# Performance work log

Measured on AMD Instinct MI355X. Metric: run time of the kernel, lower is better.

The kernel has to match this reference:

```python
import jax, jax.numpy as jnp
import numpy as np

N = 100000      # nodes
E = 1600000     # edges (before self-loops)
DIM = 128       # input feature dim
H = 5           # attention heads
C = 10          # per-head output channels
G = 256         # graphs in batch
NEG_SLOPE = 0.2 # PyG GATConv default


def setup_inputs() -> dict:
    key = jax.random.key(0)
    ks = jax.random.split(key, 8)
    x = jax.random.normal(ks[0], (N, DIM), jnp.float32)
    edge_index = jax.random.randint(ks[1], (2, E), 0, N, dtype=jnp.int64)
    batch = jnp.sort(jax.random.randint(ks[2], (N,), 0, G, dtype=jnp.int64))
    W = jax.random.normal(ks[3], (DIM, H * C), jnp.float32) * 0.05
    att_src = jax.random.normal(ks[4], (H, C), jnp.float32) * 0.1
    att_dst = jax.random.normal(ks[5], (H, C), jnp.float32) * 0.1
    bias = jnp.zeros((H * C,), jnp.float32)
    lin_w = jax.random.normal(ks[6], (H * C, 1), jnp.float32) * 0.1
    lin_b = jnp.zeros((1,), jnp.float32)
    return {"x": x, "W": W, "att_src": att_src, "att_dst": att_dst,
            "bias": bias, "lin_w": lin_w, "lin_b": lin_b,
            "edge_index": edge_index, "batch": batch}


def reference(x, W, att_src, att_dst, bias, lin_w, lin_b, edge_index, batch):
    n = x.shape[0]
    # PyG GATConv adds self-loops by default
    loop = jnp.arange(n, dtype=edge_index.dtype)
    src = jnp.concatenate([edge_index[0], loop])  # message sources j
    dst = jnp.concatenate([edge_index[1], loop])  # message targets i

    xw = (x @ W).reshape(n, H, C)                       # [N,H,C]
    a_src = jnp.einsum('nhc,hc->nh', xw, att_src)       # [N,H]
    a_dst = jnp.einsum('nhc,hc->nh', xw, att_dst)       # [N,H]

    logits = jax.nn.leaky_relu(a_src[src] + a_dst[dst], NEG_SLOPE)  # [Etot,H]
    # segment softmax over incoming edges per target node
    m = jax.ops.segment_max(logits, dst, num_segments=n)
    ex = jnp.exp(logits - m[dst])
    denom = jax.ops.segment_sum(ex, dst, num_segments=n)
    alpha = ex / denom[dst]                              # [Etot,H]

    msg = alpha[:, :, None] * xw[src]                    # [Etot,H,C]
    out = jax.ops.segment_sum(msg, dst, num_segments=n).reshape(n, H * C) + bias
    out = jax.nn.elu(out)                                # [N,H*C]

    # global_mean_pool over graph ids
    gsum = jax.ops.segment_sum(out, batch, num_segments=G)
    cnt = jax.ops.segment_sum(jnp.ones((n,), out.dtype), batch, num_segments=G)
    h = gsum / jnp.maximum(cnt, 1.0)[:, None]            # [G,H*C]

    # dropout p=0.5 is identity at inference (training=False)
    y = jax.nn.sigmoid(h @ lin_w + lin_b)                # [G,1]
    return (h, y)
```

## Files before the change

### kernel.cpp

```cpp
#include <hip/hip_runtime.h>
#include <hip/hip_bf16.h>
#include <hip/hip_fp8.h>
#include <math.h>

#define DIM 128
#define H 5
#define C 10
#define HC 50
#define NG 256
#define NEG_SLOPE 0.2f
#define UNR 8
#define WP 136
#define LOG2E 1.4426950408889634f

#define BSH 6
#define NB 1563
#define SB_CAP 1344
#define B1_BLOCKS 196
#define B1_CHUNK 8192

#define BKN2 32
#define ROWS_LDS2 (BKN2 * 64)

typedef short short8 __attribute__((ext_vector_type(8)));
typedef float floatx4 __attribute__((ext_vector_type(4)));
typedef float floatx2 __attribute__((ext_vector_type(2)));

__device__ inline short f2bf(float f) {
  __hip_bfloat16 h = __float2bfloat16(f);
  return *reinterpret_cast<short*>(&h);
}
#if __has_builtin(__builtin_amdgcn_cvt_f32_fp8)
__device__ inline float fp8tof(int b) { return __builtin_amdgcn_cvt_f32_fp8(b, 0); }
#else
__device__ inline float fp8tof(int b) {
  __hip_fp8_e4m3 v;
  v.__x = (__hip_fp8_storage_t)b;
  return (float)v;
}
#endif
#if __has_builtin(__builtin_amdgcn_cvt_pk_f32_fp8)
__device__ inline floatx2 fp8pk2(int us) {
  return __builtin_amdgcn_cvt_pk_f32_fp8(us, false);
}
#else
__device__ inline floatx2 fp8pk2(int us) {
  floatx2 r;
  r.x = fp8tof(us & 0xff);
  r.y = fp8tof((us >> 8) & 0xff);
  return r;
}
#endif
#if __has_builtin(__builtin_amdgcn_exp2f)
__device__ inline float fexp2(float x) { return __builtin_amdgcn_exp2f(x); }
#else
__device__ inline float fexp2(float x) { return exp2f(x); }
#endif
#if __has_builtin(__builtin_amdgcn_cvt_pk_fp8_f32)
__device__ inline unsigned ftofp8pk(float a, float b) {
  return (unsigned)__builtin_amdgcn_cvt_pk_fp8_f32(a, b, 0, false) & 0xffffu;
}
__device__ inline unsigned char ftofp8(float f) {
  return (unsigned char)(ftofp8pk(f, f) & 0xff);
}
#else
__device__ inline unsigned char ftofp8(float f) {
  __hip_fp8_e4m3 v(f);
  return v.__x;
}
__device__ inline unsigned ftofp8pk(float a, float b) {
  return (unsigned)ftofp8(a) | ((unsigned)ftofp8(b) << 8);
}
#endif

__global__ void k_zero(int* __restrict__ g, unsigned char* __restrict__ recb,
                       int n) {
  int t = blockIdx.x * blockDim.x + threadIdx.x;
  if (t < NB) g[t] = 0;
  if (blockIdx.x == 1 && threadIdx.x < 64)
    recb[((size_t)n << 6) + threadIdx.x] = (threadIdx.x < HC) ? 0x00 : 0xFE;
}

__global__ __launch_bounds__(256) void k_work(
    const int* __restrict__ src, const int* __restrict__ dst,
    int* __restrict__ gcur, int* __restrict__ seg,
    const float* __restrict__ x, const float* __restrict__ W,
    const float* __restrict__ att_src, const float* __restrict__ att_dst,
    unsigned char* __restrict__ recb, __hip_bfloat16* __restrict__ adst,
    int E_, int n) {
  __shared__ __align__(16) char smem[NB * 3 * sizeof(int)];
  int tid = threadIdx.x;
  if (blockIdx.x < B1_BLOCKS) {
    int* hist = (int*)smem;
    int* curs = hist + NB;
    int* baser = curs + NB;
    for (int i = tid; i < NB; i += 256) hist[i] = 0;
    __syncthreads();
    int e0 = blockIdx.x * B1_CHUNK;
    int dreg[32];
#pragma unroll
    for (int k = 0; k < 32; ++k) {
      int e = e0 + (k << 8) + tid;
      dreg[k] = (e < E_) ? dst[e] : -1;
      if (dreg[k] >= 0) atomicAdd(&hist[((unsigned)dreg[k]) >> BSH], 1);
    }
    __syncthreads();
    for (int i = tid; i < NB; i += 256) {
      baser[i] = hist[i] ? atomicAdd(&gcur[i], hist[i]) : 0;
      curs[i] = 0;
    }
    __syncthreads();
#pragma unroll
    for (int k = 0; k < 32; ++k) {
      if (dreg[k] >= 0) {
        int d = dreg[k];
        int s = ((unsigned)d) >> BSH;
        int pos = baser[s] + atomicAdd(&curs[s], 1);
        if (pos < SB_CAP)
          seg[(size_t)s * SB_CAP + pos] = (src[e0 + (k << 8) + tid] << 6) | (d & 63);
      }
    }
    return;
  }
  short* swt = (short*)smem;
  {
    int k = tid & 127;
    if (tid < 128) {
      for (int j = 0; j < HC; ++j) swt[j * WP + k] = f2bf(W[k * HC + j]);
    } else {
      float sv[H] = {0.f, 0.f, 0.f, 0.f, 0.f};
      float dv[H] = {0.f, 0.f, 0.f, 0.f, 0.f};
#pragma unroll
      for (int c = 0; c < HC; ++c) {
        float w = W[k * HC + c];
        sv[c / C] += w * att_src[c];
        dv[c / C] += w * att_dst[c];
      }
#pragma unroll
      for (int h = 0; h < H; ++h) {
        swt[(HC + h) * WP + k] = f2bf(sv[h] * LOG2E);
        swt[(55 + h) * WP + k] = f2bf(dv[h] * LOG2E);
      }
      for (int j = 60; j < 64; ++j) swt[j * WP + k] = 0;
    }
  }
  __syncthreads();
  int wv = tid >> 6, lane = tid & 63;
  int tiles = (n + 15) >> 4;
  int tile = (blockIdx.x - B1_BLOCKS) * 4 + wv;
  if (tile >= tiles) return;
  int r = lane & 15, q = lane >> 4;
  int node = tile * 16 + r;
  const float* xr = x + (size_t)min(node, n - 1) * DIM + q * 8;
  floatx4 acc[4];
#pragma unroll
  for (int nt = 0; nt < 4; ++nt) acc[nt] = (floatx4){0.f, 0.f, 0.f, 0.f};
#pragma unroll
  for (int ks = 0; ks < 4; ++ks) {
    float4 a0 = *(const float4*)(xr + ks * 32);
    float4 a1 = *(const float4*)(xr + ks * 32 + 4);
    short8 bx;
    bx[0] = f2bf(a0.x); bx[1] = f2bf(a0.y); bx[2] = f2bf(a0.z); bx[3] = f2bf(a0.w);
    bx[4] = f2bf(a1.x); bx[5] = f2bf(a1.y); bx[6] = f2bf(a1.z); bx[7] = f2bf(a1.w);
    const short* wb = &swt[r * WP + q * 8 + ks * 32];
    short8 w0 = *(const short8*)(wb);
    short8 w1 = *(const short8*)(wb + 16 * WP);
    short8 w2 = *(const short8*)(wb + 32 * WP);
    short8 w3 = *(const short8*)(wb + 48 * WP);
    acc[0] = __builtin_amdgcn_mfma_f32_16x16x32_bf16(w0, bx, acc[0], 0, 0, 0);
    acc[1] = __builtin_amdgcn_mfma_f32_16x16x32_bf16(w1, bx, acc[1], 0, 0, 0);
    acc[2] = __builtin_amdgcn_mfma_f32_16x16x32_bf16(w2, bx, acc[2], 0, 0, 0);
    acc[3] = __builtin_amdgcn_mfma_f32_16x16x32_bf16(w3, bx, acc[3], 0, 0, 0);
  }
  float xa = __shfl_up(acc[3][3], 16);
  float xb = __shfl_up(acc[3][1], 16);
  float xc = __shfl_up(acc[3][2], 16);
  if (node < n) {
    size_t base = (size_t)node << 6;
#pragma unroll
    for (int nt = 0; nt < 3; ++nt) {
      unsigned d = ftofp8pk(acc[nt][0], acc[nt][1]) |
                   (ftofp8pk(acc[nt][2], acc[nt][3]) << 16);
      *(unsigned*)(recb + base + nt * 16 + (q << 2)) = d;
    }
    unsigned d;
    if (q == 0) {
      d = ftofp8pk(acc[3][0], acc[3][1]) | (ftofp8pk(acc[3][2], acc[3][2]) << 16);
    } else if (q == 1) {
      d = ftofp8pk(xa, xa) | (ftofp8pk(acc[3][0], acc[3][0]) << 16);
      adst[(size_t)node * H + 0] = __float2bfloat16(acc[3][3]);
    } else if (q == 2) {
      d = ftofp8pk(xb, xb) | (ftofp8pk(xc, xc) << 16);
      adst[(size_t)node * H + 1] = __float2bfloat16(acc[3][0]);
      adst[(size_t)node * H + 2] = __float2bfloat16(acc[3][1]);
      adst[(size_t)node * H + 3] = __float2bfloat16(acc[3][2]);
      adst[(size_t)node * H + 4] = __float2bfloat16(acc[3][3]);
    } else {
      d = 0;
    }
    *(unsigned*)(recb + base + 48 + (q << 2)) = d;
  }
}

__global__ __launch_bounds__(256) void k_bin_gat(
    const int* __restrict__ seg, const int* __restrict__ gcur,
    const unsigned char* __restrict__ recb, const __hip_bfloat16* __restrict__ adst,
    const float* __restrict__ bias, float* __restrict__ out_node, int n) {
  __shared__ int rows[ROWS_LDS2];
  __shared__ __align__(16) int wbuf[4][128];
  int tid = threadIdx.x;
  int blk = blockIdx.x;
  int b = blk >> 1;
  int half32 = blk & 1;
  int lo = (b << BSH) + (half32 << 5);
  int hi = min(lo + BKN2, n);
  for (int k = tid; k < ROWS_LDS2; k += 256) rows[k] = n;
  __syncthreads();
  int cnt = min(gcur[b], SB_CAP);
  for (int k = tid; k < cnt; k += 256) {
    int e = seg[(size_t)b * SB_CAP + k];
    int dl = e & 63;
    if ((dl >> 5) == half32) {
      int s = ((unsigned)e) >> 6;
      int base = (dl & 31) << 6;
      int off = s & 63;
      int old = atomicExch(&rows[base + off], s);
      int probes = 0;
      while (old != n && probes < 128) {
        off = (off + 1) & 63;
        old = atomicExch(&rows[base + off], old);
        ++probes;
      }
    }
  }
  __syncthreads();

  int w = tid >> 6, lane = tid & 63;
  int* wb = wbuf[w];
  int nn = hi - lo;
  int pairsN = (nn + 1) >> 1;
  int hl = lane & 31;
  int hf = lane >> 5;
  bool chl = hl < 25;
  int h = hl / 5;
  int bpidx = ((hf << 5) + 25 + h) << 2;
  unsigned rowoff = (unsigned)(hl << 1);
  int rbase = hf << 6;

  for (int pr = w; pr < pairsN; pr += 4) {
    int i0l = pr * 2;
    int i1l = min(i0l + 1, nn - 1);
    int i0 = lo + i0l, i1 = lo + i1l;
    int iown = hf ? i1 : i0;
    float adi = 0.f;
    if (chl) adi = __bfloat162float(adst[(size_t)iown * H + h]);

    int jraw0 = rows[(i0l << 6) | lane];
    int jraw1 = rows[(i1l << 6) | lane];
    ((int2*)wb)[lane] = make_int2(n, n);
    bool v0 = (unsigned)jraw0 < (unsigned)n;
    unsigned long long mk0 = __ballot(v0);
    int deg0 = __popcll(mk0);
    int bel0 = __popcll(mk0 & ((1ull << lane) - 1ull));
    if (v0) wb[bel0] = jraw0;
    bool v1 = (unsigned)jraw1 < (unsigned)n;
    unsigned long long mk1 = __ballot(v1);
    int deg1 = __popcll(mk1);
    int bel1 = __popcll(mk1 & ((1ull << lane) - 1ull));
    if (v1) wb[64 + bel1] = jraw1;
    int mx = max(deg0, deg1);

    float dpA, dpB = 0.f, a0A, a0B = 0.f, a1A, a1B = 0.f;
    {
      int us = *(const unsigned short*)(recb + (((size_t)(unsigned)iown << 6) | rowoff));
      int asv = __builtin_amdgcn_ds_bpermute(bpidx, us);
      float asi = fp8tof(asv);
      float z = asi + adi;
      z = fmaxf(z, NEG_SLOPE * z);
      float pw = fexp2(z);
      floatx2 f = fp8pk2(us);
      dpA = pw;
      a0A = pw * f.x;
      a1A = pw * f.y;
    }
    for (int s0 = 0; s0 < mx; s0 += UNR) {
      int2 jp[UNR / 2];
#pragma unroll
      for (int up = 0; up < UNR / 2; ++up)
        jp[up] = *(const int2*)&wb[rbase + s0 + up * 2];
#pragma unroll
      for (int u = 0; u < UNR; ++u) {
        unsigned j = (unsigned)((u & 1) ? jp[u >> 1].y : jp[u >> 1].x);
        int us = *(const unsigned short*)(recb + (((size_t)j << 6) | rowoff));
        int asv = __builtin_amdgcn_ds_bpermute(bpidx, us);
        float asi = fp8tof(asv);
        float z = asi + adi;
        z = fmaxf(z, NEG_SLOPE * z);
        float pw = fexp2(z);
        floatx2 f = fp8pk2(us);
        if (u & 1) {
          dpB += pw;
          a0B = fmaf(pw, f.x, a0B);
          a1B = fmaf(pw, f.y, a1B);
        } else {
          dpA += pw;
          a0A = fmaf(pw, f.x, a0A);
          a1A = fmaf(pw, f.y, a1A);
        }
      }
    }
    if (chl) {
      float dp = dpA + dpB;
      float a0 = a0A + a0B, a1 = a1A + a1B;
      int c0 = hl * 2;
      float o0 = a0 / dp + bias[c0];
      o0 = o0 > 0.f ? o0 : __expf(o0) - 1.f;
      float o1 = a1 / dp + bias[c0 + 1];
      o1 = o1 > 0.f ? o1 : __expf(o1) - 1.f;
      float2 st;
      st.x = o0;
      st.y = o1;
      *(float2*)(out_node + (size_t)iown * HC + c0) = st;
    }
  }
}

__global__ __launch_bounds__(1024) void k_pool(
    const float* __restrict__ out_node, const int* __restrict__ batch,
    const float* __restrict__ lin_w, const float* __restrict__ lin_b,
    float* __restrict__ out, int n) {
  __shared__ int sb[2];
  __shared__ float sacc[16][HC];
  int g = blockIdx.x;
  int t = threadIdx.x;
  if (t < 2) {
    int target = g + t, lo = 0, hi = n;
    while (lo < hi) {
      int mid = (lo + hi) >> 1;
      if (batch[mid] < target) lo = mid + 1; else hi = mid;
    }
    sb[t] = lo;
  }
  __syncthreads();
  int s = sb[0], e = sb[1];
  int w = t >> 6, lane = t & 63;
  float a = 0.f;
  if (lane < HC)
    for (int i = s + w; i < e; i += 16) a += out_node[(size_t)i * HC + lane];
  if (lane < HC) sacc[w][lane] = a;
  __syncthreads();
  if (t < HC) {
    float r0 = 0.f, r1 = 0.f, r2 = 0.f, r3 = 0.f;
#pragma unroll
    for (int k = 0; k < 4; ++k) {
      r0 += sacc[k][t];
      r1 += sacc[4 + k][t];
      r2 += sacc[8 + k][t];
      r3 += sacc[12 + k][t];
    }
    float hv = ((r0 + r1) + (r2 + r3)) / fmaxf((float)(e - s), 1.f);
    out[g * HC + t] = hv;
    sacc[0][t] = hv * lin_w[t];
  }
  __syncthreads();
  if (t == 0) {
    float p = 0.f;
    for (int c = 0; c < HC; ++c) p += sacc[0][c];
    out[NG * HC + g] = 1.f / (1.f + __expf(-(p + lin_b[0])));
  }
}

extern "C" void kernel_launch(void* const* d_in, const int* in_sizes, int n_in,
                              void* d_out, int out_size, void* d_ws, size_t ws_size,
                              hipStream_t stream) {
  const float* x       = (const float*)d_in[0];
  const float* W       = (const float*)d_in[1];
  const float* att_src = (const float*)d_in[2];
  const float* att_dst = (const float*)d_in[3];
  const float* bias    = (const float*)d_in[4];
  const float* lin_w   = (const float*)d_in[5];
  const float* lin_b   = (const float*)d_in[6];
  const int*   eidx    = (const int*)d_in[7];
  const int*   batch   = (const int*)d_in[8];

  int n  = in_sizes[0] / DIM;
  int E_ = in_sizes[7] / 2;
  const int* srcp = eidx;
  const int* dstp = eidx + E_;

  char* p = (char*)d_ws;
  float* out_node = (float*)p; p += (size_t)n * HC * sizeof(float);
  unsigned char* recb = (unsigned char*)p; p += (size_t)(n + 1) * 64;
  __hip_bfloat16* adst = (__hip_bfloat16*)p; p += (size_t)n * H * sizeof(__hip_bfloat16);
  p = (char*)(((uintptr_t)p + 255) & ~(uintptr_t)255);
  int* gcur = (int*)p; p += NB * sizeof(int);
  p = (char*)(((uintptr_t)p + 255) & ~(uintptr_t)255);
  int* seg = (int*)p; p += (size_t)NB * SB_CAP * sizeof(int);

  float* out = (float*)d_out;

  int tiles = (n + 15) / 16;
  int mfma_blocks = (tiles + 3) / 4;
  int nbk2 = (n + BKN2 - 1) / BKN2;

  k_zero<<<2, 1024, 0, stream>>>(gcur, recb, n);
  k_work<<<B1_BLOCKS + mfma_blocks, 256, 0, stream>>>(
      srcp, dstp, gcur, seg, x, W, att_src, att_dst, recb, adst, E_, n);
  k_bin_gat<<<nbk2, 256, 0, stream>>>(seg, gcur, recb, adst, bias, out_node, n);
  k_pool<<<NG, 1024, 0, stream>>>(out_node, batch, lin_w, lin_b, out, n);
}
```

Baseline: 200.6 us.

## Replace global-atomic bucket cursors with per-block fixed-slot bucket storage

The edge binning pass no longer reserves space in each bucket with global atomics on a shared cursor array. Each binning block now writes its edges into private fixed-size slots per bucket, along with a per-block count, and the number of binning blocks is doubled with half-size chunks. The aggregation kernel then walks every block's slot list for its bucket. This removes global atomic contention and the need to zero the counters, but adds many scattered small reads in the aggregation kernel, a much larger sparse segment buffer, and silently drops edges when a block puts more than the slot count into one bucket.

```diff
diff --git a/kernel.cpp b/kernel.cpp
--- a/kernel.cpp
+++ b/kernel.cpp
@@ -15,9 +15,9 @@
 
 #define BSH 6
 #define NB 1563
-#define SB_CAP 1344
-#define B1_BLOCKS 196
-#define B1_CHUNK 8192
+#define B1_BLOCKS 391
+#define B1_CHUNK 4096
+#define SLOTS 24
 
 #define BKN2 32
 #define ROWS_LDS2 (BKN2 * 64)
@@ -73,51 +73,46 @@
 }
 #endif
 
-__global__ void k_zero(int* __restrict__ g, unsigned char* __restrict__ recb,
-                       int n) {
-  int t = blockIdx.x * blockDim.x + threadIdx.x;
-  if (t < NB) g[t] = 0;
-  if (blockIdx.x == 1 && threadIdx.x < 64)
+__global__ void k_zero(unsigned char* __restrict__ recb, int n) {
+  if (threadIdx.x < 64)
     recb[((size_t)n << 6) + threadIdx.x] = (threadIdx.x < HC) ? 0x00 : 0xFE;
 }
 
 __global__ __launch_bounds__(256) void k_work(
     const int* __restrict__ src, const int* __restrict__ dst,
-    int* __restrict__ gcur, int* __restrict__ seg,
+    int* __restrict__ cnts, int* __restrict__ seg,
     const float* __restrict__ x, const float* __restrict__ W,
     const float* __restrict__ att_src, const float* __restrict__ att_dst,
     unsigned char* __restrict__ recb, __hip_bfloat16* __restrict__ adst,
     int E_, int n) {
-  __shared__ __align__(16) char smem[NB * 3 * sizeof(int)];
+  __shared__ __align__(16) char smem[64 * WP * sizeof(short)];
   int tid = threadIdx.x;
   if (blockIdx.x < B1_BLOCKS) {
     int* hist = (int*)smem;
-    int* curs = hist + NB;
-    int* baser = curs + NB;
+    int blk = blockIdx.x;
     for (int i = tid; i < NB; i += 256) hist[i] = 0;
     __syncthreads();
-    int e0 = blockIdx.x * B1_CHUNK;
-    int dreg[32];
-#pragma unroll
-    for (int k = 0; k < 32; ++k) {
+    int e0 = blk * B1_CHUNK;
+    int dreg[16];
+#pragma unroll
+    for (int k = 0; k < 16; ++k) {
       int e = e0 + (k << 8) + tid;
       dreg[k] = (e < E_) ? dst[e] : -1;
       if (dreg[k] >= 0) atomicAdd(&hist[((unsigned)dreg[k]) >> BSH], 1);
     }
     __syncthreads();
-    for (int i = tid; i < NB; i += 256) {
-      baser[i] = hist[i] ? atomicAdd(&gcur[i], hist[i]) : 0;
-      curs[i] = 0;
-    }
+    for (int i = tid; i < NB; i += 256)
+      cnts[blk * NB + i] = min(hist[i], SLOTS);
     __syncthreads();
 #pragma unroll
-    for (int k = 0; k < 32; ++k) {
+    for (int k = 0; k < 16; ++k) {
       if (dreg[k] >= 0) {
         int d = dreg[k];
         int s = ((unsigned)d) >> BSH;
-        int pos = baser[s] + atomicAdd(&curs[s], 1);
-        if (pos < SB_CAP)
-          seg[(size_t)s * SB_CAP + pos] = (src[e0 + (k << 8) + tid] << 6) | (d & 63);
+        int pos = atomicAdd(&hist[s], -1) - 1;
+        if (pos >= 0 && pos < SLOTS)
+          seg[(size_t)(blk * NB + s) * SLOTS + pos] =
+              (src[e0 + (k << 8) + tid] << 6) | (d & 63);
       }
     }
     return;
@@ -203,7 +198,7 @@
 }
 
 __global__ __launch_bounds__(256) void k_bin_gat(
-    const int* __restrict__ seg, const int* __restrict__ gcur,
+    const int* __restrict__ cnts, const int* __restrict__ seg,
     const unsigned char* __restrict__ recb, const __hip_bfloat16* __restrict__ adst,
     const float* __restrict__ bias, float* __restrict__ out_node, int n) {
   __shared__ int rows[ROWS_LDS2];
@@ -216,20 +211,23 @@
   int hi = min(lo + BKN2, n);
   for (int k = tid; k < ROWS_LDS2; k += 256) rows[k] = n;
   __syncthreads();
-  int cnt = min(gcur[b], SB_CAP);
-  for (int k = tid; k < cnt; k += 256) {
-    int e = seg[(size_t)b * SB_CAP + k];
-    int dl = e & 63;
-    if ((dl >> 5) == half32) {
-      int s = ((unsigned)e) >> 6;
-      int base = (dl & 31) << 6;
-      int off = s & 63;
-      int old = atomicExch(&rows[base + off], s);
-      int probes = 0;
-      while (old != n && probes < 128) {
-        off = (off + 1) & 63;
-        old = atomicExch(&rows[base + off], old);
-        ++probes;
+  for (int rb = tid; rb < B1_BLOCKS; rb += 256) {
+    int c = cnts[rb * NB + b];
+    size_t sb = (size_t)(rb * NB + b) * SLOTS;
+    for (int i = 0; i < c; ++i) {
+      int e = seg[sb + i];
+      int dl = e & 63;
+      if ((dl >> 5) == half32) {
+        int s = ((unsigned)e) >> 6;
+        int base = (dl & 31) << 6;
+        int off = s & 63;
+        int old = atomicExch(&rows[base + off], s);
+        int probes = 0;
+        while (old != n && probes < 128) {
+          off = (off + 1) & 63;
+          old = atomicExch(&rows[base + off], old);
+          ++probes;
+        }
       }
     }
   }
@@ -393,9 +391,9 @@
   unsigned char* recb = (unsigned char*)p; p += (size_t)(n + 1) * 64;
   __hip_bfloat16* adst = (__hip_bfloat16*)p; p += (size_t)n * H * sizeof(__hip_bfloat16);
   p = (char*)(((uintptr_t)p + 255) & ~(uintptr_t)255);
-  int* gcur = (int*)p; p += NB * sizeof(int);
+  int* cnts = (int*)p; p += (size_t)B1_BLOCKS * NB * sizeof(int);
   p = (char*)(((uintptr_t)p + 255) & ~(uintptr_t)255);
-  int* seg = (int*)p; p += (size_t)NB * SB_CAP * sizeof(int);
+  int* seg = (int*)p; p += (size_t)B1_BLOCKS * NB * SLOTS * sizeof(int);
 
   float* out = (float*)d_out;
 
@@ -403,9 +401,9 @@
   int mfma_blocks = (tiles + 3) / 4;
   int nbk2 = (n + BKN2 - 1) / BKN2;
 
-  k_zero<<<2, 1024, 0, stream>>>(gcur, recb, n);
+  k_zero<<<1, 64, 0, stream>>>(recb, n);
   k_work<<<B1_BLOCKS + mfma_blocks, 256, 0, stream>>>(
-      srcp, dstp, gcur, seg, x, W, att_src, att_dst, recb, adst, E_, n);
-  k_bin_gat<<<nbk2, 256, 0, stream>>>(seg, gcur, recb, adst, bias, out_node, n);
+      srcp, dstp, cnts, seg, x, W, att_src, att_dst, recb, adst, E_, n);
+  k_bin_gat<<<nbk2, 256, 0, stream>>>(cnts, seg, recb, adst, bias, out_node, n);
   k_pool<<<NG, 1024, 0, stream>>>(out_node, batch, lin_w, lin_b, out, n);
 }
```

Measured after the change: 231.1 us. 15.2% more time.

## Shard edge bucket counters four ways and halve binning chunk size

Applied to the files above, without the earlier changes.

Edge binning now writes into four sub-buckets per destination bucket, picked by block index, each with its own global counter. This spreads global atomics across more addresses and doubles the number of binning blocks, each handling half as many edges, for more parallelism. The consumer kernel now walks four sub-segments per bucket. Each shard has a capacity of 336, so a skewed shard can overflow and silently drop edges where the single shared capacity before would not.

```diff
diff --git a/kernel.cpp b/kernel.cpp
--- a/kernel.cpp
+++ b/kernel.cpp
@@ -15,9 +15,10 @@
 
 #define BSH 6
 #define NB 1563
-#define SB_CAP 1344
-#define B1_BLOCKS 196
-#define B1_CHUNK 8192
+#define B1_BLOCKS 391
+#define B1_CHUNK 4096
+#define NSH 4
+#define SCAP 336
 
 #define BKN2 32
 #define ROWS_LDS2 (BKN2 * 64)
@@ -76,9 +77,8 @@
 __global__ void k_zero(int* __restrict__ g, unsigned char* __restrict__ recb,
                        int n) {
   int t = blockIdx.x * blockDim.x + threadIdx.x;
-  if (t < NB) g[t] = 0;
-  if (blockIdx.x == 1 && threadIdx.x < 64)
-    recb[((size_t)n << 6) + threadIdx.x] = (threadIdx.x < HC) ? 0x00 : 0xFE;
+  if (t < NSH * NB) g[t] = 0;
+  if (t < 64) recb[((size_t)n << 6) + t] = (t < HC) ? 0x00 : 0xFE;
 }
 
 __global__ __launch_bounds__(256) void k_work(
@@ -96,28 +96,31 @@
     int* baser = curs + NB;
     for (int i = tid; i < NB; i += 256) hist[i] = 0;
     __syncthreads();
-    int e0 = blockIdx.x * B1_CHUNK;
-    int dreg[32];
-#pragma unroll
-    for (int k = 0; k < 32; ++k) {
+    int blk = blockIdx.x;
+    int e0 = blk * B1_CHUNK;
+    int sh = blk & (NSH - 1);
+    int dreg[16];
+#pragma unroll
+    for (int k = 0; k < 16; ++k) {
       int e = e0 + (k << 8) + tid;
       dreg[k] = (e < E_) ? dst[e] : -1;
       if (dreg[k] >= 0) atomicAdd(&hist[((unsigned)dreg[k]) >> BSH], 1);
     }
     __syncthreads();
     for (int i = tid; i < NB; i += 256) {
-      baser[i] = hist[i] ? atomicAdd(&gcur[i], hist[i]) : 0;
+      baser[i] = hist[i] ? atomicAdd(&gcur[sh * NB + i], hist[i]) : 0;
       curs[i] = 0;
     }
     __syncthreads();
 #pragma unroll
-    for (int k = 0; k < 32; ++k) {
+    for (int k = 0; k < 16; ++k) {
       if (dreg[k] >= 0) {
         int d = dreg[k];
         int s = ((unsigned)d) >> BSH;
         int pos = baser[s] + atomicAdd(&curs[s], 1);
-        if (pos < SB_CAP)
-          seg[(size_t)s * SB_CAP + pos] = (src[e0 + (k << 8) + tid] << 6) | (d & 63);
+        if (pos < SCAP)
+          seg[((size_t)s * NSH + sh) * SCAP + pos] =
+              (src[e0 + (k << 8) + tid] << 6) | (d & 63);
       }
     }
     return;
@@ -216,20 +219,24 @@
   int hi = min(lo + BKN2, n);
   for (int k = tid; k < ROWS_LDS2; k += 256) rows[k] = n;
   __syncthreads();
-  int cnt = min(gcur[b], SB_CAP);
-  for (int k = tid; k < cnt; k += 256) {
-    int e = seg[(size_t)b * SB_CAP + k];
-    int dl = e & 63;
-    if ((dl >> 5) == half32) {
-      int s = ((unsigned)e) >> 6;
-      int base = (dl & 31) << 6;
-      int off = s & 63;
-      int old = atomicExch(&rows[base + off], s);
-      int probes = 0;
-      while (old != n && probes < 128) {
-        off = (off + 1) & 63;
-        old = atomicExch(&rows[base + off], old);
-        ++probes;
+#pragma unroll
+  for (int sh = 0; sh < NSH; ++sh) {
+    int cnt = min(gcur[sh * NB + b], SCAP);
+    size_t sb = ((size_t)b * NSH + sh) * SCAP;
+    for (int k = tid; k < cnt; k += 256) {
+      int e = seg[sb + k];
+      int dl = e & 63;
+      if ((dl >> 5) == half32) {
+        int s = ((unsigned)e) >> 6;
+        int base = (dl & 31) << 6;
+        int off = s & 63;
+        int old = atomicExch(&rows[base + off], s);
+        int probes = 0;
+        while (old != n && probes < 128) {
+          off = (off + 1) & 63;
+          old = atomicExch(&rows[base + off], old);
+          ++probes;
+        }
       }
     }
   }
@@ -393,9 +400,9 @@
   unsigned char* recb = (unsigned char*)p; p += (size_t)(n + 1) * 64;
   __hip_bfloat16* adst = (__hip_bfloat16*)p; p += (size_t)n * H * sizeof(__hip_bfloat16);
   p = (char*)(((uintptr_t)p + 255) & ~(uintptr_t)255);
-  int* gcur = (int*)p; p += NB * sizeof(int);
+  int* gcur = (int*)p; p += (size_t)NSH * NB * sizeof(int);
   p = (char*)(((uintptr_t)p + 255) & ~(uintptr_t)255);
-  int* seg = (int*)p; p += (size_t)NB * SB_CAP * sizeof(int);
+  int* seg = (int*)p; p += (size_t)NB * NSH * SCAP * sizeof(int);
 
   float* out = (float*)d_out;
 
@@ -403,7 +410,7 @@
   int mfma_blocks = (tiles + 3) / 4;
   int nbk2 = (n + BKN2 - 1) / BKN2;
 
-  k_zero<<<2, 1024, 0, stream>>>(gcur, recb, n);
+  k_zero<<<7, 1024, 0, stream>>>(gcur, recb, n);
   k_work<<<B1_BLOCKS + mfma_blocks, 256, 0, stream>>>(
       srcp, dstp, gcur, seg, x, W, att_src, att_dst, recb, adst, E_, n);
   k_bin_gat<<<nbk2, 256, 0, stream>>>(seg, gcur, recb, adst, bias, out_node, n);
```

Measured after the change: 182.0 us. 9.3% less time.
